# Kernel tuning notes

Hardware: AMD Instinct MI355X
Metric: run time of the kernel (lower is better)

## Reference

```python
import jax, jax.numpy as jnp
import numpy as np

B, S, D = 16, 8192, 256  # batch, seq_len, feature dim (== hdims)
HDIMS, HEADS = 256, 8
NEG_BIG = 1e12


def setup_inputs() -> dict:
    key = jax.random.key(0)
    k1, k2, k3 = jax.random.split(key, 3)
    x = jax.random.normal(k1, (B, S, D), dtype=jnp.float32)
    mask = jnp.ones((B, S), dtype=jnp.bool_)
    # glorot-ish scaling for stability
    k_kernel = jax.random.normal(k2, (D, HDIMS), dtype=jnp.float32) * (1.0 / np.sqrt(D))
    o_kernel = jax.random.normal(k3, (HDIMS, HEADS), dtype=jnp.float32) * (1.0 / np.sqrt(HDIMS))
    return {"x": x, "mask": mask, "k_kernel": k_kernel, "o_kernel": o_kernel}


def reference(x, mask, k_kernel, o_kernel):
    # scores: Dense(tanh) -> Dense(heads), shape (B, S, HEADS)
    w = jnp.tanh(x @ k_kernel) @ o_kernel
    m = mask.astype(jnp.float32)[..., None]            # (B, S, 1)
    w = w - (1.0 - m) * NEG_BIG
    w = jax.nn.softmax(w, axis=1)                      # softmax over sequence
    # fused weighted-sum pooling: avoids (B,S,H,D) broadcast intermediate
    pooled = jnp.einsum('bsh,bsd->bhd', w, x)          # (B, HEADS, D)
    return pooled.reshape(x.shape[0], HEADS * HDIMS)   # (B, HEADS*HDIMS)
```

## Files before the change

### kernel.cpp

```cpp
#include <hip/hip_runtime.h>

#define S_LEN 8192
#define DIM   256
#define CHUNK 512
#define TB    64
#define NIT   8
#define NBLK  256

typedef __attribute__((ext_vector_type(8))) short          short8;
typedef __attribute__((ext_vector_type(4))) unsigned short u16x4;
typedef __attribute__((ext_vector_type(4))) unsigned int   u32x4;
typedef __attribute__((ext_vector_type(4))) float          f32x4;
typedef __attribute__((ext_vector_type(8))) __bf16         bf16x8;

static __device__ __forceinline__ unsigned short f2bf(float f){
  unsigned int u = __builtin_bit_cast(unsigned int, f);
  u = (u + 0x7fffu + ((u >> 16) & 1u)) >> 16;
  return (unsigned short)u;
}
static __device__ __forceinline__ float bf2f(unsigned short h){
  unsigned int u = ((unsigned int)h) << 16;
  return __builtin_bit_cast(float, u);
}
static __device__ __forceinline__ float fast_tanh(float x){
  float e = __expf(2.0f * x);
  return 1.0f - 2.0f / (e + 1.0f);
}
static __device__ __forceinline__ f32x4 mfma_bf16(short8 a, short8 b, f32x4 c){
  return __builtin_amdgcn_mfma_f32_16x16x32_bf16(
      __builtin_bit_cast(bf16x8, a), __builtin_bit_cast(bf16x8, b), c, 0, 0, 0);
}
static __device__ __forceinline__ void softbar(){
  asm volatile("s_waitcnt lgkmcnt(0)\n\ts_barrier" ::: "memory");
}

__global__ void k_prep(const float* __restrict__ kk, unsigned short* __restrict__ KT){
  int idx = blockIdx.x * 512 + threadIdx.x;
  int n = idx >> 8, k = idx & 255;
  KT[(n << 8) + k] = f2bf(kk[(k << 8) + n]);
}


__global__ __launch_bounds__(512, 2) void k_main(
    const float* __restrict__ x, const int* __restrict__ mask,
    const float* __restrict__ ok, const unsigned short* __restrict__ KT,
    float* __restrict__ ACC, float* __restrict__ ML)
{
  __shared__ __align__(16) unsigned char sXB [32768];
  __shared__ __align__(16) unsigned char sXT2[32768];
  __shared__ __align__(16) unsigned char sT2 [32768];
  __shared__ __align__(16) unsigned char sOT [16*528];
  __shared__ __align__(16) unsigned char sPT [16*144];
  __shared__ float sWMax[4][16];
  __shared__ float sWSum[4][16];
  __shared__ float sMrun[16];
  __shared__ float sLrun[16];
  __shared__ float sFsc[16];
  __shared__ float sMaskB[CHUNK];

  const int tid = threadIdx.x;
  const int w   = tid >> 6;
  const int l   = tid & 63;
  const int l15 = l & 15;
  const int lhi = l >> 4;
  const int bid = blockIdx.x;
  const int b   = bid >> 4;
  const int chunk0 = (bid & 15) * CHUNK;

  for (int idx = tid; idx < 16 * 256; idx += 512){
    int h = idx >> 8, k = idx & 255;
    float v = (h < 8) ? ok[k * 8 + h] : 0.0f;
    *(unsigned short*)(sOT + h * 528 + k * 2) = f2bf(v);
  }
  if (tid < 16){ sMrun[tid] = -1e30f; sLrun[tid] = 0.0f; }
  sMaskB[tid] = mask[(size_t)b * S_LEN + chunk0 + tid] ? 0.0f : 1e12f;

  short8 aF[2][8];
  #pragma unroll
  for (int mi = 0; mi < 2; ++mi){
    int hidA = l15 + ((2*w + mi) << 4);
    #pragma unroll
    for (int k = 0; k < 8; ++k){
      int col = (k << 5) + (lhi << 3);
      aF[mi][k] = *(const short8*)((const unsigned char*)KT + (((size_t)hidA << 8) + col) * 2);
    }
  }

  const unsigned char* xb = (const unsigned char*)(x + ((size_t)b * S_LEN + chunk0) * DIM);

  f32x4 xr[8];
  #pragma unroll
  for (int q = 0; q < 8; ++q)
    xr[q] = *(const f32x4*)(xb + (((size_t)(8*w + q)) * DIM + 4*l) * 4);

  f32x4 acc3[2];
  acc3[0] = (f32x4){0.f,0.f,0.f,0.f};
  acc3[1] = acc3[0];

  __syncthreads();

  for (int it = 0; it < NIT; ++it){
    unsigned vd[8][2];
    #pragma unroll
    for (int q = 0; q < 8; ++q){
      vd[q][0] = (unsigned)f2bf(xr[q][0]) | ((unsigned)f2bf(xr[q][1]) << 16);
      vd[q][1] = (unsigned)f2bf(xr[q][2]) | ((unsigned)f2bf(xr[q][3]) << 16);
    }
    {
      int dblk = l >> 2;
      #pragma unroll
      for (int q = 0; q < 8; ++q){
        int r = 8*w + q;
        int srow = r ^ (dblk & 3);
        int off = ((l & 3) * 8) ^ (((srow >> 2) & 1) << 4);
        *(uint2*)(sXB + dblk * 2048 + srow * 32 + off) = make_uint2(vd[q][0], vd[q][1]);
      }
      #pragma unroll
      for (int i = 0; i < 4; ++i){
        int h = i >> 1;
        unsigned dwv[4];
        #pragma unroll
        for (int j = 0; j < 4; ++j){
          unsigned a = vd[2*j][h], c = vd[2*j+1][h];
          dwv[j] = (i & 1) ? ((a >> 16) | (c & 0xFFFF0000u))
                           : ((a & 0xFFFFu) | (c << 16));
        }
        int d = 4*l + i;
        int key = ((d & 3) << 1) ^ ((d >> 2) & 7);
        *(u32x4*)(sXT2 + d * 128 + ((16*w) ^ (key << 4))) =
            (u32x4){dwv[0], dwv[1], dwv[2], dwv[3]};
      }
    }
    if (it + 1 < NIT){
      #pragma unroll
      for (int q = 0; q < 8; ++q)
        xr[q] = *(const f32x4*)(xb + (((size_t)((it+1)*TB + 8*w + q)) * DIM + 4*l) * 4);
    }
    softbar();

    #pragma unroll
    for (int nt = 0; nt < 4; ++nt){
      int row = l15 + (nt << 4);
      f32x4 a0 = (f32x4){0.f,0.f,0.f,0.f};
      f32x4 a1 = a0;
      #pragma unroll
      for (int k8 = 0; k8 < 8; ++k8){
        int dblkR = k8 * 2 + (lhi >> 1);
        int srowB = row ^ (dblkR & 3);
        int off = ((lhi & 1) * 16) ^ (((srowB >> 2) & 1) << 4);
        short8 bF = *(const short8*)(sXB + dblkR * 2048 + srowB * 32 + off);
        a0 = mfma_bf16(aF[0][k8], bF, a0);
        a1 = mfma_bf16(aF[1][k8], bF, a1);
      }
      #pragma unroll
      for (int mi = 0; mi < 2; ++mi){
        f32x4 av = mi ? a1 : a0;
        u16x4 tv;
        #pragma unroll
        for (int r = 0; r < 4; ++r) tv[r] = f2bf(fast_tanh(av[r]));
        int hidb2 = ((((2*w + mi) << 4) + (lhi << 2))) * 2;
        *(u16x4*)(sT2 + row * 512 + (hidb2 ^ ((row & 7) << 4))) = tv;
      }
    }
    softbar();

    float sc[4];
    if (w < 4){
      int row = l15 + (w << 4);
      f32x4 a2 = (f32x4){0.f,0.f,0.f,0.f};
      #pragma unroll
      for (int k = 0; k < 8; ++k){
        int col2 = (k << 6) + (lhi << 4);
        short8 aT = *(const short8*)(sT2 + row * 512 + (col2 ^ ((row & 7) << 4)));
        short8 bO = *(const short8*)(sOT + l15 * 528 + col2);
        a2 = mfma_bf16(aT, bO, a2);
      }
      int rbase = (w << 4) + (lhi << 2);
      #pragma unroll
      for (int r = 0; r < 4; ++r)
        sc[r] = a2[r] - sMaskB[it * TB + rbase + r];
      float vm = fmaxf(fmaxf(sc[0], sc[1]), fmaxf(sc[2], sc[3]));
      vm = fmaxf(vm, __shfl_xor(vm, 16));
      vm = fmaxf(vm, __shfl_xor(vm, 32));
      if (l < 16) sWMax[w][l] = vm;
    }
    softbar();

    float m_old = sMrun[l15];
    float wm = fmaxf(fmaxf(sWMax[0][l15], sWMax[1][l15]),
                     fmaxf(sWMax[2][l15], sWMax[3][l15]));
    float m_new = fmaxf(m_old, wm);
    float fsc = __expf(m_old - m_new);
    if (w == 0 && l < 16) sFsc[l] = fsc;
    if (w < 4){
      float psum = 0.0f;
      int rbase = (w << 4) + (lhi << 2);
      #pragma unroll
      for (int r = 0; r < 4; ++r){
        float p = __expf(sc[r] - m_new);
        unsigned short pb = f2bf(p);
        psum += bf2f(pb);
        *(unsigned short*)(sPT + l15 * 144 + (rbase + r) * 2) = pb;
      }
      psum += __shfl_xor(psum, 16);
      psum += __shfl_xor(psum, 32);
      if (l < 16) sWSum[w][l] = psum;
    }
    softbar();

    #pragma unroll
    for (int r = 0; r < 4; ++r){
      float fr = sFsc[(lhi << 2) + r];
      acc3[0][r] *= fr;
      acc3[1][r] *= fr;
    }
    short8 aP0 = *(const short8*)(sPT + l15 * 144 + lhi * 16);
    short8 aP1 = *(const short8*)(sPT + l15 * 144 + 64 + lhi * 16);
    #pragma unroll
    for (int mi = 0; mi < 2; ++mi){
      int d = (2*w + mi) * 16 + l15;
      int key = ((d & 3) << 1) ^ ((d >> 2) & 7);
      const unsigned char* pd = sXT2 + d * 128;
      short8 b0 = *(const short8*)(pd + (((lhi * 16)      ) ^ (key << 4)));
      short8 b1 = *(const short8*)(pd + ((64 + lhi * 16) ^ (key << 4)));
      acc3[mi] = mfma_bf16(aP0, b0, acc3[mi]);
      acc3[mi] = mfma_bf16(aP1, b1, acc3[mi]);
    }
    if (w == 0 && l < 16){
      sLrun[l] = sLrun[l] * fsc + sWSum[0][l] + sWSum[1][l] + sWSum[2][l] + sWSum[3][l];
      sMrun[l] = m_new;
    }
    softbar();
  }

  if (lhi < 2){
    #pragma unroll
    for (int mi = 0; mi < 2; ++mi){
      int d = ((2*w + mi) << 4) + l15;
      #pragma unroll
      for (int r = 0; r < 4; ++r){
        int h = (lhi << 2) + r;
        ACC[((size_t)bid * 8 + h) * 256 + d] = acc3[mi][r];
      }
    }
  }
  if (w == 0 && l < 8){
    ML[bid * 16 + l]     = sMrun[l];
    ML[bid * 16 + 8 + l] = sLrun[l];
  }
}

__global__ void k_merge(const float* __restrict__ ACC, const float* __restrict__ ML,
                        float* __restrict__ out){
  int b = blockIdx.x >> 3;
  int h = blockIdx.x & 7;
  int d = threadIdx.x;
  float M = -1e30f;
  #pragma unroll
  for (int c = 0; c < 16; ++c) M = fmaxf(M, ML[(b * 16 + c) * 16 + h]);
  float L = 0.0f, V = 0.0f;
  #pragma unroll 4
  for (int c = 0; c < 16; ++c){
    int blk = b * 16 + c;
    float e = __expf(ML[blk * 16 + h] - M);
    L += e * ML[blk * 16 + 8 + h];
    V += e * ACC[((size_t)blk * 8 + h) * 256 + d];
  }
  out[(size_t)b * 2048 + h * 256 + d] = V / L;
}

extern "C" void kernel_launch(void* const* d_in, const int* in_sizes, int n_in,
                              void* d_out, int out_size, void* d_ws, size_t ws_size,
                              hipStream_t stream){
  const float* x   = (const float*)d_in[0];
  const int*  mask = (const int*) d_in[1];
  const float* kk  = (const float*)d_in[2];
  const float* ok  = (const float*)d_in[3];
  float* out = (float*)d_out;

  unsigned short* KT = (unsigned short*)d_ws;
  float* ACC = (float*)((char*)d_ws + 131072);
  float* ML  = (float*)((char*)d_ws + 131072 + 2097152);

  k_prep <<<128, 512, 0, stream>>>(kk, KT);
  k_main <<<NBLK, 512, 0, stream>>>(x, mask, ok, KT, ACC, ML);
  k_merge<<<128, 256, 0, stream>>>(ACC, ML, out);
}
```

Measured before the change: 59.83 us.

## Double block to 1024 threads, splitting rows and K across wave halves

```diff
diff --git a/kernel.cpp b/kernel.cpp
--- a/kernel.cpp
+++ b/kernel.cpp
@@ -9,7 +9,6 @@
 
 typedef __attribute__((ext_vector_type(8))) short          short8;
 typedef __attribute__((ext_vector_type(4))) unsigned short u16x4;
-typedef __attribute__((ext_vector_type(4))) unsigned int   u32x4;
 typedef __attribute__((ext_vector_type(4))) float          f32x4;
 typedef __attribute__((ext_vector_type(8))) __bf16         bf16x8;
 
@@ -41,7 +40,7 @@
 }
 
 
-__global__ __launch_bounds__(512, 2) void k_main(
+__global__ __launch_bounds__(1024, 4) void k_main(
     const float* __restrict__ x, const int* __restrict__ mask,
     const float* __restrict__ ok, const unsigned short* __restrict__ KT,
     float* __restrict__ ACC, float* __restrict__ ML)
@@ -60,6 +59,8 @@
 
   const int tid = threadIdx.x;
   const int w   = tid >> 6;
+  const int wh  = w & 7;
+  const int wr  = w >> 3;
   const int l   = tid & 63;
   const int l15 = l & 15;
   const int lhi = l >> 4;
@@ -67,18 +68,19 @@
   const int b   = bid >> 4;
   const int chunk0 = (bid & 15) * CHUNK;
 
-  for (int idx = tid; idx < 16 * 256; idx += 512){
+  for (int idx = tid; idx < 16 * 256; idx += 1024){
     int h = idx >> 8, k = idx & 255;
     float v = (h < 8) ? ok[k * 8 + h] : 0.0f;
     *(unsigned short*)(sOT + h * 528 + k * 2) = f2bf(v);
   }
   if (tid < 16){ sMrun[tid] = -1e30f; sLrun[tid] = 0.0f; }
-  sMaskB[tid] = mask[(size_t)b * S_LEN + chunk0 + tid] ? 0.0f : 1e12f;
+  if (tid < CHUNK)
+    sMaskB[tid] = mask[(size_t)b * S_LEN + chunk0 + tid] ? 0.0f : 1e12f;
 
   short8 aF[2][8];
   #pragma unroll
   for (int mi = 0; mi < 2; ++mi){
-    int hidA = l15 + ((2*w + mi) << 4);
+    int hidA = l15 + ((2*wh + mi) << 4);
     #pragma unroll
     for (int k = 0; k < 8; ++k){
       int col = (k << 5) + (lhi << 3);
@@ -88,10 +90,10 @@
 
   const unsigned char* xb = (const unsigned char*)(x + ((size_t)b * S_LEN + chunk0) * DIM);
 
-  f32x4 xr[8];
+  f32x4 xr[4];
   #pragma unroll
-  for (int q = 0; q < 8; ++q)
-    xr[q] = *(const f32x4*)(xb + (((size_t)(8*w + q)) * DIM + 4*l) * 4);
+  for (int q = 0; q < 4; ++q)
+    xr[q] = *(const f32x4*)(xb + (((size_t)(4*w + q)) * DIM + 4*l) * 4);
 
   f32x4 acc3[2];
   acc3[0] = (f32x4){0.f,0.f,0.f,0.f};
@@ -100,17 +102,17 @@
   __syncthreads();
 
   for (int it = 0; it < NIT; ++it){
-    unsigned vd[8][2];
-    #pragma unroll
-    for (int q = 0; q < 8; ++q){
+    unsigned vd[4][2];
+    #pragma unroll
+    for (int q = 0; q < 4; ++q){
       vd[q][0] = (unsigned)f2bf(xr[q][0]) | ((unsigned)f2bf(xr[q][1]) << 16);
       vd[q][1] = (unsigned)f2bf(xr[q][2]) | ((unsigned)f2bf(xr[q][3]) << 16);
     }
     {
       int dblk = l >> 2;
       #pragma unroll
-      for (int q = 0; q < 8; ++q){
-        int r = 8*w + q;
+      for (int q = 0; q < 4; ++q){
+        int r = 4*w + q;
         int srow = r ^ (dblk & 3);
         int off = ((l & 3) * 8) ^ (((srow >> 2) & 1) << 4);
         *(uint2*)(sXB + dblk * 2048 + srow * 32 + off) = make_uint2(vd[q][0], vd[q][1]);
@@ -118,28 +120,28 @@
       #pragma unroll
       for (int i = 0; i < 4; ++i){
         int h = i >> 1;
-        unsigned dwv[4];
-        #pragma unroll
-        for (int j = 0; j < 4; ++j){
-          unsigned a = vd[2*j][h], c = vd[2*j+1][h];
-          dwv[j] = (i & 1) ? ((a >> 16) | (c & 0xFFFF0000u))
-                           : ((a & 0xFFFFu) | (c << 16));
+        unsigned dw0, dw1;
+        {
+          unsigned a = vd[0][h], c = vd[1][h];
+          dw0 = (i & 1) ? ((a >> 16) | (c & 0xFFFF0000u)) : ((a & 0xFFFFu) | (c << 16));
+          a = vd[2][h]; c = vd[3][h];
+          dw1 = (i & 1) ? ((a >> 16) | (c & 0xFFFF0000u)) : ((a & 0xFFFFu) | (c << 16));
         }
         int d = 4*l + i;
         int key = ((d & 3) << 1) ^ ((d >> 2) & 7);
-        *(u32x4*)(sXT2 + d * 128 + ((16*w) ^ (key << 4))) =
-            (u32x4){dwv[0], dwv[1], dwv[2], dwv[3]};
+        *(uint2*)(sXT2 + d * 128 + ((8*w) ^ (key << 4))) = make_uint2(dw0, dw1);
       }
     }
     if (it + 1 < NIT){
       #pragma unroll
-      for (int q = 0; q < 8; ++q)
-        xr[q] = *(const f32x4*)(xb + (((size_t)((it+1)*TB + 8*w + q)) * DIM + 4*l) * 4);
-    }
-    softbar();
-
-    #pragma unroll
-    for (int nt = 0; nt < 4; ++nt){
+      for (int q = 0; q < 4; ++q)
+        xr[q] = *(const f32x4*)(xb + (((size_t)((it+1)*TB + 4*w + q)) * DIM + 4*l) * 4);
+    }
+    softbar();
+
+    #pragma unroll
+    for (int nt2 = 0; nt2 < 2; ++nt2){
+      int nt  = wr * 2 + nt2;
       int row = l15 + (nt << 4);
       f32x4 a0 = (f32x4){0.f,0.f,0.f,0.f};
       f32x4 a1 = a0;
@@ -158,7 +160,7 @@
         u16x4 tv;
         #pragma unroll
         for (int r = 0; r < 4; ++r) tv[r] = f2bf(fast_tanh(av[r]));
-        int hidb2 = ((((2*w + mi) << 4) + (lhi << 2))) * 2;
+        int hidb2 = ((((2*wh + mi) << 4) + (lhi << 2))) * 2;
         *(u16x4*)(sT2 + row * 512 + (hidb2 ^ ((row & 7) << 4))) = tv;
       }
     }
@@ -214,17 +216,15 @@
       acc3[0][r] *= fr;
       acc3[1][r] *= fr;
     }
-    short8 aP0 = *(const short8*)(sPT + l15 * 144 + lhi * 16);
-    short8 aP1 = *(const short8*)(sPT + l15 * 144 + 64 + lhi * 16);
-    #pragma unroll
-    for (int mi = 0; mi < 2; ++mi){
-      int d = (2*w + mi) * 16 + l15;
-      int key = ((d & 3) << 1) ^ ((d >> 2) & 7);
-      const unsigned char* pd = sXT2 + d * 128;
-      short8 b0 = *(const short8*)(pd + (((lhi * 16)      ) ^ (key << 4)));
-      short8 b1 = *(const short8*)(pd + ((64 + lhi * 16) ^ (key << 4)));
-      acc3[mi] = mfma_bf16(aP0, b0, acc3[mi]);
-      acc3[mi] = mfma_bf16(aP1, b1, acc3[mi]);
+    {
+      short8 aP = *(const short8*)(sPT + l15 * 144 + wr * 64 + lhi * 16);
+      #pragma unroll
+      for (int mi = 0; mi < 2; ++mi){
+        int d = (2*wh + mi) * 16 + l15;
+        int key = ((d & 3) << 1) ^ ((d >> 2) & 7);
+        short8 bX = *(const short8*)(sXT2 + d * 128 + ((wr * 64 + lhi * 16) ^ (key << 4)));
+        acc3[mi] = mfma_bf16(aP, bX, acc3[mi]);
+      }
     }
     if (w == 0 && l < 16){
       sLrun[l] = sLrun[l] * fsc + sWSum[0][l] + sWSum[1][l] + sWSum[2][l] + sWSum[3][l];
@@ -233,14 +233,21 @@
     softbar();
   }
 
-  if (lhi < 2){
+  if (wr == 1){
+    #pragma unroll
+    for (int mi = 0; mi < 2; ++mi)
+      *(f32x4*)(sXB + (((2*wh + mi) << 6) + l) * 16) = acc3[mi];
+  }
+  __syncthreads();
+  if (wr == 0 && lhi < 2){
     #pragma unroll
     for (int mi = 0; mi < 2; ++mi){
-      int d = ((2*w + mi) << 4) + l15;
+      f32x4 other = *(const f32x4*)(sXB + (((2*wh + mi) << 6) + l) * 16);
+      int d = ((2*wh + mi) << 4) + l15;
       #pragma unroll
       for (int r = 0; r < 4; ++r){
         int h = (lhi << 2) + r;
-        ACC[((size_t)bid * 8 + h) * 256 + d] = acc3[mi][r];
+        ACC[((size_t)bid * 8 + h) * 256 + d] = acc3[mi][r] + other[r];
       }
     }
   }
@@ -283,6 +290,6 @@
   float* ML  = (float*)((char*)d_ws + 131072 + 2097152);
 
   k_prep <<<128, 512, 0, stream>>>(kk, KT);
-  k_main <<<NBLK, 512, 0, stream>>>(x, mask, ok, KT, ACC, ML);
+  k_main <<<NBLK, 1024, 0, stream>>>(x, mask, ok, KT, ACC, ML);
   k_merge<<<128, 256, 0, stream>>>(ACC, ML, out);
 }
```

New measurement: 115.5 us. 1.93x slower.

## Split main kernel into score pass then exact-softmax pooling pass over chunk

Applied to the files above, without the earlier changes.

```diff
diff --git a/kernel.cpp b/kernel.cpp
--- a/kernel.cpp
+++ b/kernel.cpp
@@ -46,16 +46,13 @@
     const float* __restrict__ ok, const unsigned short* __restrict__ KT,
     float* __restrict__ ACC, float* __restrict__ ML)
 {
-  __shared__ __align__(16) unsigned char sXB [32768];
-  __shared__ __align__(16) unsigned char sXT2[32768];
-  __shared__ __align__(16) unsigned char sT2 [32768];
+  __shared__ __align__(16) unsigned char sX  [32768];
+  __shared__ __align__(16) unsigned char sT2P[32768];
+  __shared__ __align__(16) unsigned char sSC [34816];
   __shared__ __align__(16) unsigned char sOT [16*528];
-  __shared__ __align__(16) unsigned char sPT [16*144];
-  __shared__ float sWMax[4][16];
-  __shared__ float sWSum[4][16];
-  __shared__ float sMrun[16];
-  __shared__ float sLrun[16];
-  __shared__ float sFsc[16];
+  __shared__ float sRed[32][16];
+  __shared__ float sM[16];
+  __shared__ float sL[16];
   __shared__ float sMaskB[CHUNK];
 
   const int tid = threadIdx.x;
@@ -72,13 +69,14 @@
     float v = (h < 8) ? ok[k * 8 + h] : 0.0f;
     *(unsigned short*)(sOT + h * 528 + k * 2) = f2bf(v);
   }
-  if (tid < 16){ sMrun[tid] = -1e30f; sLrun[tid] = 0.0f; }
   sMaskB[tid] = mask[(size_t)b * S_LEN + chunk0 + tid] ? 0.0f : 1e12f;
 
-  short8 aF[2][8];
+  const int h4 = w & 3;
+  const int rh = w >> 2;
+  short8 aF[4][8];
   #pragma unroll
-  for (int mi = 0; mi < 2; ++mi){
-    int hidA = l15 + ((2*w + mi) << 4);
+  for (int mi = 0; mi < 4; ++mi){
+    int hidA = l15 + ((4*h4 + mi) << 4);
     #pragma unroll
     for (int k = 0; k < 8; ++k){
       int col = (k << 5) + (lhi << 3);
@@ -93,10 +91,6 @@
   for (int q = 0; q < 8; ++q)
     xr[q] = *(const f32x4*)(xb + (((size_t)(8*w + q)) * DIM + 4*l) * 4);
 
-  f32x4 acc3[2];
-  acc3[0] = (f32x4){0.f,0.f,0.f,0.f};
-  acc3[1] = acc3[0];
-
   __syncthreads();
 
   for (int it = 0; it < NIT; ++it){
@@ -113,22 +107,7 @@
         int r = 8*w + q;
         int srow = r ^ (dblk & 3);
         int off = ((l & 3) * 8) ^ (((srow >> 2) & 1) << 4);
-        *(uint2*)(sXB + dblk * 2048 + srow * 32 + off) = make_uint2(vd[q][0], vd[q][1]);
-      }
-      #pragma unroll
-      for (int i = 0; i < 4; ++i){
-        int h = i >> 1;
-        unsigned dwv[4];
-        #pragma unroll
-        for (int j = 0; j < 4; ++j){
-          unsigned a = vd[2*j][h], c = vd[2*j+1][h];
-          dwv[j] = (i & 1) ? ((a >> 16) | (c & 0xFFFF0000u))
-                           : ((a & 0xFFFFu) | (c << 16));
-        }
-        int d = 4*l + i;
-        int key = ((d & 3) << 1) ^ ((d >> 2) & 7);
-        *(u32x4*)(sXT2 + d * 128 + ((16*w) ^ (key << 4))) =
-            (u32x4){dwv[0], dwv[1], dwv[2], dwv[3]};
+        *(uint2*)(sX + dblk * 2048 + srow * 32 + off) = make_uint2(vd[q][0], vd[q][1]);
       }
     }
     if (it + 1 < NIT){
@@ -139,96 +118,145 @@
     softbar();
 
     #pragma unroll
-    for (int nt = 0; nt < 4; ++nt){
-      int row = l15 + (nt << 4);
+    for (int nt2 = 0; nt2 < 2; ++nt2){
+      int row = l15 + ((2*rh + nt2) << 4);
       f32x4 a0 = (f32x4){0.f,0.f,0.f,0.f};
-      f32x4 a1 = a0;
+      f32x4 a1 = a0, a2v = a0, a3 = a0;
       #pragma unroll
       for (int k8 = 0; k8 < 8; ++k8){
         int dblkR = k8 * 2 + (lhi >> 1);
         int srowB = row ^ (dblkR & 3);
         int off = ((lhi & 1) * 16) ^ (((srowB >> 2) & 1) << 4);
-        short8 bF = *(const short8*)(sXB + dblkR * 2048 + srowB * 32 + off);
-        a0 = mfma_bf16(aF[0][k8], bF, a0);
-        a1 = mfma_bf16(aF[1][k8], bF, a1);
-      }
-      #pragma unroll
-      for (int mi = 0; mi < 2; ++mi){
-        f32x4 av = mi ? a1 : a0;
+        short8 bF = *(const short8*)(sX + dblkR * 2048 + srowB * 32 + off);
+        a0  = mfma_bf16(aF[0][k8], bF, a0);
+        a1  = mfma_bf16(aF[1][k8], bF, a1);
+        a2v = mfma_bf16(aF[2][k8], bF, a2v);
+        a3  = mfma_bf16(aF[3][k8], bF, a3);
+      }
+      f32x4 av[4] = {a0, a1, a2v, a3};
+      #pragma unroll
+      for (int mi = 0; mi < 4; ++mi){
         u16x4 tv;
         #pragma unroll
-        for (int r = 0; r < 4; ++r) tv[r] = f2bf(fast_tanh(av[r]));
-        int hidb2 = ((((2*w + mi) << 4) + (lhi << 2))) * 2;
-        *(u16x4*)(sT2 + row * 512 + (hidb2 ^ ((row & 7) << 4))) = tv;
-      }
-    }
-    softbar();
-
-    float sc[4];
+        for (int r = 0; r < 4; ++r) tv[r] = f2bf(fast_tanh(av[mi][r]));
+        int hidb2 = ((((4*h4 + mi) << 4) + (lhi << 2))) * 2;
+        *(u16x4*)(sT2P + row * 512 + (hidb2 ^ ((row & 7) << 4))) = tv;
+      }
+    }
+    softbar();
+
     if (w < 4){
       int row = l15 + (w << 4);
       f32x4 a2 = (f32x4){0.f,0.f,0.f,0.f};
       #pragma unroll
       for (int k = 0; k < 8; ++k){
         int col2 = (k << 6) + (lhi << 4);
-        short8 aT = *(const short8*)(sT2 + row * 512 + (col2 ^ ((row & 7) << 4)));
+        short8 aT = *(const short8*)(sT2P + row * 512 + (col2 ^ ((row & 7) << 4)));
         short8 bO = *(const short8*)(sOT + l15 * 528 + col2);
         a2 = mfma_bf16(aT, bO, a2);
       }
       int rbase = (w << 4) + (lhi << 2);
       #pragma unroll
-      for (int r = 0; r < 4; ++r)
-        sc[r] = a2[r] - sMaskB[it * TB + rbase + r];
-      float vm = fmaxf(fmaxf(sc[0], sc[1]), fmaxf(sc[2], sc[3]));
-      vm = fmaxf(vm, __shfl_xor(vm, 16));
-      vm = fmaxf(vm, __shfl_xor(vm, 32));
-      if (l < 16) sWMax[w][l] = vm;
-    }
-    softbar();
-
-    float m_old = sMrun[l15];
-    float wm = fmaxf(fmaxf(sWMax[0][l15], sWMax[1][l15]),
-                     fmaxf(sWMax[2][l15], sWMax[3][l15]));
-    float m_new = fmaxf(m_old, wm);
-    float fsc = __expf(m_old - m_new);
-    if (w == 0 && l < 16) sFsc[l] = fsc;
-    if (w < 4){
-      float psum = 0.0f;
-      int rbase = (w << 4) + (lhi << 2);
-      #pragma unroll
       for (int r = 0; r < 4; ++r){
-        float p = __expf(sc[r] - m_new);
-        unsigned short pb = f2bf(p);
-        psum += bf2f(pb);
-        *(unsigned short*)(sPT + l15 * 144 + (rbase + r) * 2) = pb;
-      }
-      psum += __shfl_xor(psum, 16);
-      psum += __shfl_xor(psum, 32);
-      if (l < 16) sWSum[w][l] = psum;
-    }
-    softbar();
-
-    #pragma unroll
-    for (int r = 0; r < 4; ++r){
-      float fr = sFsc[(lhi << 2) + r];
-      acc3[0][r] *= fr;
-      acc3[1][r] *= fr;
-    }
-    short8 aP0 = *(const short8*)(sPT + l15 * 144 + lhi * 16);
-    short8 aP1 = *(const short8*)(sPT + l15 * 144 + 64 + lhi * 16);
-    #pragma unroll
-    for (int mi = 0; mi < 2; ++mi){
-      int d = (2*w + mi) * 16 + l15;
+        float sc = a2[r] - sMaskB[it * TB + rbase + r];
+        *(float*)(sSC + (it * TB + rbase + r) * 68 + l15 * 4) = sc;
+      }
+    }
+    softbar();
+  }
+
+  #pragma unroll
+  for (int q = 0; q < 8; ++q)
+    xr[q] = *(const f32x4*)(xb + (((size_t)(8*w + q)) * DIM + 4*l) * 4);
+
+  {
+    int seg = tid >> 4, head = tid & 15;
+    float m = -1e30f;
+    #pragma unroll
+    for (int j = 0; j < 16; ++j)
+      m = fmaxf(m, *(const float*)(sSC + (seg * 16 + j) * 68 + head * 4));
+    sRed[seg][head] = m;
+  }
+  softbar();
+  if (tid < 16){
+    float m = -1e30f;
+    #pragma unroll
+    for (int s = 0; s < 32; ++s) m = fmaxf(m, sRed[s][tid]);
+    sM[tid] = m;
+  }
+  softbar();
+  {
+    int head = tid >> 5, rseg = tid & 31;
+    float M = sM[head];
+    float psum = 0.0f;
+    unsigned pk[8];
+    #pragma unroll
+    for (int jj = 0; jj < 8; ++jj){
+      float s0 = *(const float*)(sSC + (rseg * 16 + 2*jj    ) * 68 + head * 4);
+      float s1 = *(const float*)(sSC + (rseg * 16 + 2*jj + 1) * 68 + head * 4);
+      unsigned short p0 = f2bf(__expf(s0 - M));
+      unsigned short p1 = f2bf(__expf(s1 - M));
+      psum += bf2f(p0) + bf2f(p1);
+      pk[jj] = (unsigned)p0 | ((unsigned)p1 << 16);
+    }
+    *(u32x4*)(sT2P + head * 1040 + rseg * 32     ) = (u32x4){pk[0],pk[1],pk[2],pk[3]};
+    *(u32x4*)(sT2P + head * 1040 + rseg * 32 + 16) = (u32x4){pk[4],pk[5],pk[6],pk[7]};
+    sRed[rseg][head] = psum;
+  }
+  softbar();
+  if (tid < 16){
+    float s = 0.0f;
+    #pragma unroll
+    for (int r = 0; r < 32; ++r) s += sRed[r][tid];
+    sL[tid] = s;
+  }
+
+  f32x4 acc3[2];
+  acc3[0] = (f32x4){0.f,0.f,0.f,0.f};
+  acc3[1] = acc3[0];
+
+  for (int it = 0; it < NIT; ++it){
+    unsigned vd[8][2];
+    #pragma unroll
+    for (int q = 0; q < 8; ++q){
+      vd[q][0] = (unsigned)f2bf(xr[q][0]) | ((unsigned)f2bf(xr[q][1]) << 16);
+      vd[q][1] = (unsigned)f2bf(xr[q][2]) | ((unsigned)f2bf(xr[q][3]) << 16);
+    }
+    #pragma unroll
+    for (int i = 0; i < 4; ++i){
+      int hh = i >> 1;
+      unsigned dwv[4];
+      #pragma unroll
+      for (int j = 0; j < 4; ++j){
+        unsigned a = vd[2*j][hh], c = vd[2*j+1][hh];
+        dwv[j] = (i & 1) ? ((a >> 16) | (c & 0xFFFF0000u))
+                         : ((a & 0xFFFFu) | (c << 16));
+      }
+      int d = 4*l + i;
       int key = ((d & 3) << 1) ^ ((d >> 2) & 7);
-      const unsigned char* pd = sXT2 + d * 128;
-      short8 b0 = *(const short8*)(pd + (((lhi * 16)      ) ^ (key << 4)));
-      short8 b1 = *(const short8*)(pd + ((64 + lhi * 16) ^ (key << 4)));
-      acc3[mi] = mfma_bf16(aP0, b0, acc3[mi]);
-      acc3[mi] = mfma_bf16(aP1, b1, acc3[mi]);
-    }
-    if (w == 0 && l < 16){
-      sLrun[l] = sLrun[l] * fsc + sWSum[0][l] + sWSum[1][l] + sWSum[2][l] + sWSum[3][l];
-      sMrun[l] = m_new;
+      *(u32x4*)(sX + d * 128 + ((16*w) ^ (key << 4))) =
+          (u32x4){dwv[0], dwv[1], dwv[2], dwv[3]};
+    }
+    if (it + 1 < NIT){
+      #pragma unroll
+      for (int q = 0; q < 8; ++q)
+        xr[q] = *(const f32x4*)(xb + (((size_t)((it+1)*TB + 8*w + q)) * DIM + 4*l) * 4);
+    }
+    softbar();
+
+    {
+      short8 aP0 = *(const short8*)(sT2P + l15 * 1040 + it * 128 +      lhi * 16);
+      short8 aP1 = *(const short8*)(sT2P + l15 * 1040 + it * 128 + 64 + lhi * 16);
+      #pragma unroll
+      for (int mi = 0; mi < 2; ++mi){
+        int d = (2*w + mi) * 16 + l15;
+        int key = ((d & 3) << 1) ^ ((d >> 2) & 7);
+        const unsigned char* pd = sX + d * 128;
+        short8 b0 = *(const short8*)(pd + (((     lhi * 16)) ^ (key << 4)));
+        short8 b1 = *(const short8*)(pd + (((64 + lhi * 16)) ^ (key << 4)));
+        acc3[mi] = mfma_bf16(aP0, b0, acc3[mi]);
+        acc3[mi] = mfma_bf16(aP1, b1, acc3[mi]);
+      }
     }
     softbar();
   }
@@ -244,9 +272,9 @@
       }
     }
   }
-  if (w == 0 && l < 8){
-    ML[bid * 16 + l]     = sMrun[l];
-    ML[bid * 16 + 8 + l] = sLrun[l];
+  if (tid < 8){
+    ML[bid * 16 + tid]     = sM[tid];
+    ML[bid * 16 + 8 + tid] = sL[tid];
   }
 }
 
```

Result: slower. 77.81 us (+30.1%).
